# Kernel tuning notes

Hardware: AMD Instinct MI355X
Metric: run time of the kernel (lower is better)

The kernel has to match this reference:

```python
import jax, jax.numpy as jnp
import numpy as np

N_HEAD = 16
POSE = 5
YAW = 1
END_X, END_Y = 18, 32
THETA = 1000.0
LN_EPS = 1e-5

def compute_axial_cis(dim, end_x, end_y, theta):
    # Axial 2D rotary: dim is per-head dim; dim//4 freqs per spatial axis.
    n = dim // 4
    freqs = 1.0 / (theta ** (jnp.arange(0, dim, 4)[:n].astype(jnp.float32) / dim))
    t = jnp.arange(end_x * end_y, dtype=jnp.float32)
    t_x = t % end_x
    t_y = jnp.floor(t / end_x)
    ang = jnp.concatenate([t_x[:, None] * freqs[None, :], t_y[:, None] * freqs[None, :]], axis=-1)  # [L, dim//2]
    return jnp.cos(ang), jnp.sin(ang)

def apply_rotary(x, cos, sin):
    # x: [B,H,L,D]; complex pairing = consecutive (even, odd) lanes, as in view_as_complex
    xe, xo = x[..., 0::2], x[..., 1::2]
    oe = xe * cos - xo * sin
    oo = xe * sin + xo * cos
    return jnp.stack([oe, oo], axis=-1).reshape(x.shape)

def layernorm(z, g, b):
    m = jnp.mean(z, axis=-1, keepdims=True)
    v = jnp.mean(jnp.square(z - m), axis=-1, keepdims=True)
    return (z - m) * jax.lax.rsqrt(v + LN_EPS) * g + b

def setup_inputs() -> dict:
    key = jax.random.key(0)
    ks = jax.random.split(key, 8)
    B, T, C = 16, 582, 1024
    x = jax.random.normal(ks[0], (B, T, C), dtype=jnp.float32)
    # additive causal mask (0 keep / -1e9 masked), as a float attn_mask
    causal = jnp.tril(jnp.ones((T, T), dtype=jnp.float32))
    attn_mask = jnp.broadcast_to(jnp.where(causal > 0, 0.0, -1e9), (B, T, T))
    s = 0.02
    Wq = jax.random.normal(ks[1], (C, C), dtype=jnp.float32) * s
    Wk = jax.random.normal(ks[2], (C, C), dtype=jnp.float32) * s
    Wv = jax.random.normal(ks[3], (C, C), dtype=jnp.float32) * s
    Wo = jax.random.normal(ks[4], (C, C), dtype=jnp.float32) * s
    q_ln_g = jnp.ones((C,), jnp.float32); q_ln_b = jnp.zeros((C,), jnp.float32)
    k_ln_g = jnp.ones((C,), jnp.float32); k_ln_b = jnp.zeros((C,), jnp.float32)
    return {"x": x, "attn_mask": attn_mask, "Wq": Wq, "Wk": Wk, "Wv": Wv, "Wo": Wo,
            "q_ln_g": q_ln_g, "q_ln_b": q_ln_b, "k_ln_g": k_ln_g, "k_ln_b": k_ln_b}

def reference(x, attn_mask, Wq, Wk, Wv, Wo, q_ln_g, q_ln_b, k_ln_g, k_ln_b):
    B, T, C = x.shape
    H = N_HEAD
    D = C // H
    q = layernorm(x @ Wq.T, q_ln_g, q_ln_b)
    k = layernorm(x @ Wk.T, k_ln_g, k_ln_b)
    v = (x @ Wv.T).reshape(B, T, H, D).transpose(0, 2, 1, 3)
    q = q.reshape(B, T, H, D).transpose(0, 2, 1, 3)
    k = k.reshape(B, T, H, D).transpose(0, 2, 1, 3)
    prefix = POSE + YAW
    if T > prefix:  # static shape condition
        cos, sin = compute_axial_cis(D, END_X, END_Y, THETA)
        L = T - prefix
        cos, sin = cos[:L], sin[:L]  # [L, D//2]
        q = jnp.concatenate([q[:, :, :prefix], apply_rotary(q[:, :, prefix:], cos, sin)], axis=2)
        k = jnp.concatenate([k[:, :, :prefix], apply_rotary(k[:, :, prefix:], cos, sin)], axis=2)
    scale = 1.0 / jnp.sqrt(jnp.float32(D))
    scores = jnp.einsum("bhqd,bhkd->bhqk", q, k) * scale + attn_mask[:, None, :, :]
    att = jax.nn.softmax(scores, axis=-1)
    y = jnp.einsum("bhqk,bhkd->bhqd", att, v)
    y = y.transpose(0, 2, 1, 3).reshape(B, T, C)
    return y @ Wo.T
```

## Files before the change

### kernel.cpp

```cpp
#include <hip/hip_runtime.h>
#include <hip/hip_bf16.h>

typedef short bf16x8 __attribute__((ext_vector_type(8)));
typedef short bf16x4 __attribute__((ext_vector_type(4)));
typedef float f32x4  __attribute__((ext_vector_type(4)));

#define LDP 72

__device__ __forceinline__ float bits2f(short u) {
  return __uint_as_float(((unsigned int)(unsigned short)u) << 16);
}
__device__ __forceinline__ short f2bits(float f) {
  __hip_bfloat16 h = __float2bfloat16(f);
  return *reinterpret_cast<short*>(&h);
}
__device__ __forceinline__ void gld16(const short* g, short* l) {
  __builtin_amdgcn_global_load_lds(
      (const __attribute__((address_space(1))) void*)g,
      (__attribute__((address_space(3))) void*)l, 16, 0, 0);
}

__global__ __launch_bounds__(256)
void cvt_x_kernel(const float* __restrict__ src, short* __restrict__ dst, long n) {
  long i = ((long)blockIdx.x * 256 + threadIdx.x) * 4;
  if (i + 3 < n) {
    float4 v = *(const float4*)(src + i);
    bf16x4 o;
    o[0] = f2bits(v.x); o[1] = f2bits(v.y); o[2] = f2bits(v.z); o[3] = f2bits(v.w);
    *(bf16x4*)(dst + i) = o;
  }
}

__global__ __launch_bounds__(256)
void cvt_w_kernel(const float* __restrict__ w0, const float* __restrict__ w1,
                  const float* __restrict__ w2, const float* __restrict__ w3,
                  short* __restrict__ dst) {
  long i = ((long)blockIdx.x * 256 + threadIdx.x) * 4;
  int sel = (int)(i >> 20);
  const float* s = (sel == 0) ? w0 : (sel == 1) ? w1 : (sel == 2) ? w2 : w3;
  long off = i & ((1L << 20) - 1);
  float4 v = *(const float4*)(s + off);
  bf16x4 o;
  o[0] = f2bits(v.x); o[1] = f2bits(v.y); o[2] = f2bits(v.z); o[3] = f2bits(v.w);
  *(bf16x4*)(dst + i) = o;
}

template<int MODE>
__global__ __launch_bounds__(256)
void gemm_nt(const short* __restrict__ A, const short* __restrict__ Bm,
             float* __restrict__ OutF, short* __restrict__ Oq,
             short* __restrict__ Ok, short* __restrict__ Ov,
             int M, int K, int N, int T, int TPAD) {
  __shared__ short As[128 * 64];
  __shared__ short Bs[128 * 64];
  const int tid = threadIdx.x;
  const int w = tid >> 6, l = tid & 63;
  const int wr = w >> 1, wc = w & 1;
  const int lg = l >> 4, lo = l & 15;

  const int R = gridDim.x, C2 = gridDim.y;
  const int d = blockIdx.y * R + blockIdx.x;
  int r, c;
  if ((R & 7) == 1 && (C2 & 7) == 0) {
    const int x = d & 7, i = d >> 3;
    const int C8 = C2 >> 3;
    const int chunk = R * C8;
    const int b9 = R >> 3;
    const int rows0 = b9 + 1;
    if (x == 0) { c = i / rows0; r = i % rows0; }
    else {
      const int nb = b9 * C2;
      if (i < nb) { c = i / b9; r = rows0 + (x - 1) * b9 + i % b9; }
      else { int p = chunk + (x - 1) * C8 + (i - nb); c = p / rows0; r = p % rows0; }
    }
  } else { r = blockIdx.x; c = blockIdx.y; }
  const long row0 = (long)r * 128;
  const long col0 = (long)c * 128;

  const short* pa[4]; const short* pb[4]; short* la[4]; short* lb[4];
#pragma unroll
  for (int j = 0; j < 4; ++j) {
    const int ch = w * 4 + j;
    const int off = ch * 1024 + l * 16;
    const int row = off >> 7;
    const int lc  = (off & 127) ^ ((row & 7) << 4);
    long ga = row0 + row; if (ga > M - 1) ga = M - 1;
    pa[j] = &A[ga * K + (lc >> 1)];
    pb[j] = &Bm[(col0 + row) * K + (lc >> 1)];
    la[j] = &As[ch * 512];
    lb[j] = &Bs[ch * 512];
  }

  f32x4 acc[4][4] = {};

  for (int kt = 0; kt < K; kt += 64) {
    __syncthreads();
#pragma unroll
    for (int j = 0; j < 4; ++j) {
      gld16(pa[j] + kt, la[j]);
      gld16(pb[j] + kt, lb[j]);
    }
    __syncthreads();
    bf16x8 af[4][2], bfr[4][2];
#pragma unroll
    for (int mi = 0; mi < 4; ++mi)
#pragma unroll
      for (int ks = 0; ks < 2; ++ks) {
        int pe = (ks * 32 + lg * 8) ^ ((lo & 7) << 3);
        af[mi][ks] = *(const bf16x8*)(&As[(wr * 64 + mi * 16 + lo) * 64 + pe]);
      }
#pragma unroll
    for (int ni = 0; ni < 4; ++ni)
#pragma unroll
      for (int ks = 0; ks < 2; ++ks) {
        int pe = (ks * 32 + lg * 8) ^ ((lo & 7) << 3);
        bfr[ni][ks] = *(const bf16x8*)(&Bs[(wc * 64 + ni * 16 + lo) * 64 + pe]);
      }
#pragma unroll
    for (int mi = 0; mi < 4; ++mi)
#pragma unroll
      for (int ni = 0; ni < 4; ++ni)
#pragma unroll
        for (int ks = 0; ks < 2; ++ks)
          acc[mi][ni] = __builtin_amdgcn_mfma_f32_16x16x32_bf16(af[mi][ks], bfr[ni][ks], acc[mi][ni], 0, 0, 0);
  }

#pragma unroll
  for (int mi = 0; mi < 4; ++mi) {
#pragma unroll
    for (int rr = 0; rr < 4; ++rr) {
      long m = row0 + wr * 64 + mi * 16 + lg * 4 + rr;
      if (m >= M) continue;
#pragma unroll
      for (int ni = 0; ni < 4; ++ni) {
        long n = col0 + wc * 64 + ni * 16 + lo;
        float v = acc[mi][ni][rr];
        if constexpr (MODE == 2) {
          OutF[m * (long)N + n] = v;
        } else {
          if (n < 1024) {
            Oq[m * 1024 + n] = f2bits(v);
          } else if (n < 2048) {
            Ok[m * 1024 + (n - 1024)] = f2bits(v);
          } else {
            long b = m / T, t = m - b * T;
            long nn = n - 2048, h = nn >> 6, dd = nn & 63;
            Ov[((b * 16 + h) * 64 + dd) * TPAD + t] = f2bits(v);
          }
        }
      }
    }
  }
}

__global__ __launch_bounds__(256)
void ln_rope_kernel(const short* __restrict__ qpre, const short* __restrict__ kpre,
                    const float* __restrict__ qg, const float* __restrict__ qb2,
                    const float* __restrict__ kg, const float* __restrict__ kb2,
                    short* __restrict__ qa, short* __restrict__ ka, int T) {
  const int row = blockIdx.x;
  const short* in; const float *g, *be; short* out;
  if (blockIdx.y == 0) { in = qpre; g = qg; be = qb2; out = qa; }
  else                 { in = kpre; g = kg; be = kb2; out = ka; }
  const int tid = threadIdx.x;
  const int c0 = tid * 4;

  bf16x4 xv = *(const bf16x4*)(&in[(long)row * 1024 + c0]);
  float xf[4];
  float s = 0.f, sq = 0.f;
#pragma unroll
  for (int i = 0; i < 4; ++i) { xf[i] = bits2f(xv[i]); s += xf[i]; sq += xf[i] * xf[i]; }
#pragma unroll
  for (int o = 1; o < 64; o <<= 1) { s += __shfl_xor(s, o); sq += __shfl_xor(sq, o); }
  __shared__ float red[8];
  const int w = tid >> 6, l = tid & 63;
  if (l == 0) { red[w] = s; red[4 + w] = sq; }
  __syncthreads();
  s  = red[0] + red[1] + red[2] + red[3];
  sq = red[4] + red[5] + red[6] + red[7];
  const float mean = s * (1.0f / 1024.0f);
  const float var  = sq * (1.0f / 1024.0f) - mean * mean;
  const float rstd = rsqrtf(var + 1e-5f);

  float4 gv = *(const float4*)(&g[c0]);
  float4 bv = *(const float4*)(&be[c0]);
  float z[4];
  z[0] = (xf[0] - mean) * rstd * gv.x + bv.x;
  z[1] = (xf[1] - mean) * rstd * gv.y + bv.y;
  z[2] = (xf[2] - mean) * rstd * gv.z + bv.z;
  z[3] = (xf[3] - mean) * rstd * gv.w + bv.w;

  const int t = row % T;
  const int p = t - 6;
  if (p >= 0) {
    const float tx = (float)(p % 18);
    const float ty = (float)(p / 18);
    const int jbase = (c0 & 63) >> 1;
#pragma unroll
    for (int q2 = 0; q2 < 2; ++q2) {
      const int jj = jbase + q2;
      const int i  = jj & 15;
      const float freq = exp2f(-(float)i * 0.6228615177913804f);
      const float ang  = ((jj < 16) ? tx : ty) * freq;
      float sv, cv;
      sincosf(ang, &sv, &cv);
      const float xe = z[q2 * 2], xo = z[q2 * 2 + 1];
      z[q2 * 2]     = xe * cv - xo * sv;
      z[q2 * 2 + 1] = xe * sv + xo * cv;
    }
  }
  const long b = row / T;
  const int h = c0 >> 6, d = c0 & 63;
  bf16x4 ov;
#pragma unroll
  for (int i = 0; i < 4; ++i) ov[i] = f2bits(z[i]);
  *(bf16x4*)(&out[(((b * 16 + h) * T) + t) * 64 + d]) = ov;
}

__global__ __launch_bounds__(256)
void attn_kernel(const short* __restrict__ Q, const short* __restrict__ Kk,
                 const short* __restrict__ Vt, short* __restrict__ Y,
                 int T, int TPAD) {
  __shared__ short Ps[4][16 * LDP];
  const int tid = threadIdx.x;
  const int w = tid >> 6, l = tid & 63, lg = l >> 4, lo = l & 15;
  const int qb = gridDim.x - 1 - blockIdx.x;
  const int bh = blockIdx.y;
  const int b = bh >> 4, h = bh & 15;
  const long qbase = (long)bh * T * 64;
  const long vbase = (long)bh * 64;
  short* Pw = &Ps[w][0];

  const long qrow_l = qb * 64 + w * 16 + lo;
  bf16x8 qf[2];
  qf[0] = *(const bf16x8*)(&Q[qbase + qrow_l * 64 + lg * 8]);
  qf[1] = *(const bf16x8*)(&Q[qbase + qrow_l * 64 + 32 + lg * 8]);

  float mrow[4], lsum[4];
  f32x4 oacc[4] = {};
#pragma unroll
  for (int r = 0; r < 4; ++r) { mrow[r] = -3e38f; lsum[r] = 0.f; }
  const float SCL = 0.125f * 1.44269504f;
  const int nkt = qb + 1;

  for (int kt = 0; kt < nkt; ++kt) {
    bf16x8 kfr[4][2], vf[4][2];
#pragma unroll
    for (int ni = 0; ni < 4; ++ni)
#pragma unroll
      for (int kk = 0; kk < 2; ++kk)
        kfr[ni][kk] = *(const bf16x8*)(&Kk[qbase + (long)(kt * 64 + ni * 16 + lo) * 64 + kk * 32 + lg * 8]);
#pragma unroll
    for (int ni = 0; ni < 4; ++ni)
#pragma unroll
      for (int kk = 0; kk < 2; ++kk)
        vf[ni][kk] = *(const bf16x8*)(&Vt[(vbase + ni * 16 + lo) * TPAD + kt * 64 + kk * 32 + lg * 8]);

    f32x4 sf[4] = {};
#pragma unroll
    for (int ni = 0; ni < 4; ++ni)
#pragma unroll
      for (int kk = 0; kk < 2; ++kk)
        sf[ni] = __builtin_amdgcn_mfma_f32_16x16x32_bf16(qf[kk], kfr[ni][kk], sf[ni], 0, 0, 0);

    float pm[4][4], tmax[4];
#pragma unroll
    for (int r = 0; r < 4; ++r) tmax[r] = -3e38f;
#pragma unroll
    for (int ni = 0; ni < 4; ++ni)
#pragma unroll
      for (int r = 0; r < 4; ++r) {
        int key  = kt * 64 + ni * 16 + lo;
        int qrow = qb * 64 + w * 16 + lg * 4 + r;
        float sv = sf[ni][r] * SCL;
        if (key > qrow || key >= T) sv = -3e38f;
        pm[ni][r] = sv;
        tmax[r] = fmaxf(tmax[r], sv);
      }
#pragma unroll
    for (int r = 0; r < 4; ++r)
#pragma unroll
      for (int o = 1; o < 16; o <<= 1) tmax[r] = fmaxf(tmax[r], __shfl_xor(tmax[r], o));

    bool need = !__all(tmax[0] <= mrow[0] && tmax[1] <= mrow[1] &&
                       tmax[2] <= mrow[2] && tmax[3] <= mrow[3]);
    if (need) {
#pragma unroll
      for (int r = 0; r < 4; ++r) {
        float mn = fmaxf(mrow[r], tmax[r]);
        float fsc = exp2f(mrow[r] - mn);
        mrow[r] = mn;
        lsum[r] *= fsc;
#pragma unroll
        for (int ni = 0; ni < 4; ++ni) oacc[ni][r] *= fsc;
      }
    }
    float psum[4] = {0.f, 0.f, 0.f, 0.f};
#pragma unroll
    for (int ni = 0; ni < 4; ++ni)
#pragma unroll
      for (int r = 0; r < 4; ++r) {
        float pv = exp2f(pm[ni][r] - mrow[r]);
        pm[ni][r] = pv;
        psum[r] += pv;
      }
#pragma unroll
    for (int r = 0; r < 4; ++r) {
#pragma unroll
      for (int o = 1; o < 16; o <<= 1) psum[r] += __shfl_xor(psum[r], o);
      lsum[r] += psum[r];
    }

#pragma unroll
    for (int ni = 0; ni < 4; ++ni)
#pragma unroll
      for (int r = 0; r < 4; ++r)
        Pw[(lg * 4 + r) * LDP + ni * 16 + lo] = f2bits(pm[ni][r]);

#pragma unroll
    for (int kk = 0; kk < 2; ++kk) {
      bf16x8 pf = *(const bf16x8*)(&Pw[lo * LDP + kk * 32 + lg * 8]);
#pragma unroll
      for (int ni = 0; ni < 4; ++ni)
        oacc[ni] = __builtin_amdgcn_mfma_f32_16x16x32_bf16(pf, vf[ni][kk], oacc[ni], 0, 0, 0);
    }
  }

#pragma unroll
  for (int r = 0; r < 4; ++r) {
    int tq = qb * 64 + w * 16 + lg * 4 + r;
    if (tq >= T) continue;
    float inv = 1.0f / lsum[r];
#pragma unroll
    for (int ni = 0; ni < 4; ++ni) {
      float o = oacc[ni][r] * inv;
      Y[((long)b * T + tq) * 1024 + h * 64 + ni * 16 + lo] = f2bits(o);
    }
  }
}

extern "C" void kernel_launch(void* const* d_in, const int* in_sizes, int n_in,
                              void* d_out, int out_size, void* d_ws, size_t ws_size,
                              hipStream_t stream) {
  const float* x   = (const float*)d_in[0];
  const float* Wq  = (const float*)d_in[2];
  const float* Wk  = (const float*)d_in[3];
  const float* Wv  = (const float*)d_in[4];
  const float* Wo  = (const float*)d_in[5];
  const float* qg  = (const float*)d_in[6];
  const float* qb2 = (const float*)d_in[7];
  const float* kg  = (const float*)d_in[8];
  const float* kb2 = (const float*)d_in[9];

  const int B = 16, T = 582, C = 1024;
  const int M = B * T;
  const int TPAD = 584;

  short* ws = (short*)d_ws;
  const long E  = (long)M * C;
  const long EV = (long)B * 16 * 64 * TPAD;
  short* xb   = ws;
  short* qpre = ws + E;
  short* kpre = ws + 2 * E;
  short* ka   = ws + 3 * E;
  short* vat  = ws + 4 * E;
  short* wb   = ws + 4 * E + EV + 1024;
  short* qa   = xb;
  short* y    = qpre;
  float* out  = (float*)d_out;
  (void)ws_size; (void)in_sizes; (void)n_in; (void)out_size;

  const long WE = 1L << 20;

  cvt_x_kernel<<<(int)(E / 4 / 256), 256, 0, stream>>>(x, xb, E);
  cvt_w_kernel<<<(int)(4 * WE / 4 / 256), 256, 0, stream>>>(Wq, Wk, Wv, Wo, wb);

  dim3 gqkv((M + 127) / 128, 3072 / 128);
  gemm_nt<3><<<gqkv, 256, 0, stream>>>(xb, wb, nullptr, qpre, kpre, vat, M, C, 3072, T, TPAD);
  ln_rope_kernel<<<dim3(M, 2), 256, 0, stream>>>(qpre, kpre, qg, qb2, kg, kb2, qa, ka, T);
  attn_kernel<<<dim3((T + 63) / 64, B * 16), 256, 0, stream>>>(qa, ka, vat, y, T, TPAD);
  dim3 gout((M + 127) / 128, C / 128);
  gemm_nt<2><<<gout, 256, 0, stream>>>(y, wb + 3 * WE, out, nullptr, nullptr, nullptr, M, C, C, T, TPAD);
}
```

Measured before the change: 293.2 us.

## Merge conversion kernels, drop GEMM tile swizzle, compute softmax row sums via MFMA

The separate x and weight bf16 conversion kernels are merged into one launch, which removes a launch and its tail. The custom XCD-aware block remapping in the GEMM is removed in favour of plain blockIdx tiling. In attention, the per-row probability sum now comes from an extra MFMA against a ones vector, replacing the shuffle reductions. The sum is taken over the bf16-rounded probabilities, which slightly changes numerics, and the GEMM may lose L2 locality from the dropped swizzle.

```diff
diff --git a/kernel.cpp b/kernel.cpp
--- a/kernel.cpp
+++ b/kernel.cpp
@@ -21,28 +21,24 @@
 }
 
 __global__ __launch_bounds__(256)
-void cvt_x_kernel(const float* __restrict__ src, short* __restrict__ dst, long n) {
+void cvt_all_kernel(const float* __restrict__ x,
+                    const float* __restrict__ w0, const float* __restrict__ w1,
+                    const float* __restrict__ w2, const float* __restrict__ w3,
+                    short* __restrict__ xb, short* __restrict__ wb, long nx) {
   long i = ((long)blockIdx.x * 256 + threadIdx.x) * 4;
-  if (i + 3 < n) {
-    float4 v = *(const float4*)(src + i);
-    bf16x4 o;
-    o[0] = f2bits(v.x); o[1] = f2bits(v.y); o[2] = f2bits(v.z); o[3] = f2bits(v.w);
-    *(bf16x4*)(dst + i) = o;
-  }
-}
-
-__global__ __launch_bounds__(256)
-void cvt_w_kernel(const float* __restrict__ w0, const float* __restrict__ w1,
-                  const float* __restrict__ w2, const float* __restrict__ w3,
-                  short* __restrict__ dst) {
-  long i = ((long)blockIdx.x * 256 + threadIdx.x) * 4;
-  int sel = (int)(i >> 20);
-  const float* s = (sel == 0) ? w0 : (sel == 1) ? w1 : (sel == 2) ? w2 : w3;
-  long off = i & ((1L << 20) - 1);
+  const float* s; short* d; long off;
+  if (i < nx) { s = x; d = xb; off = i; }
+  else {
+    long j = i - nx;
+    int sel = (int)(j >> 20);
+    s = (sel == 0) ? w0 : (sel == 1) ? w1 : (sel == 2) ? w2 : w3;
+    d = wb + (j & ~((1L << 20) - 1));
+    off = j & ((1L << 20) - 1);
+  }
   float4 v = *(const float4*)(s + off);
   bf16x4 o;
   o[0] = f2bits(v.x); o[1] = f2bits(v.y); o[2] = f2bits(v.z); o[3] = f2bits(v.w);
-  *(bf16x4*)(dst + i) = o;
+  *(bf16x4*)(d + off) = o;
 }
 
 template<int MODE>
@@ -57,25 +53,8 @@
   const int w = tid >> 6, l = tid & 63;
   const int wr = w >> 1, wc = w & 1;
   const int lg = l >> 4, lo = l & 15;
-
-  const int R = gridDim.x, C2 = gridDim.y;
-  const int d = blockIdx.y * R + blockIdx.x;
-  int r, c;
-  if ((R & 7) == 1 && (C2 & 7) == 0) {
-    const int x = d & 7, i = d >> 3;
-    const int C8 = C2 >> 3;
-    const int chunk = R * C8;
-    const int b9 = R >> 3;
-    const int rows0 = b9 + 1;
-    if (x == 0) { c = i / rows0; r = i % rows0; }
-    else {
-      const int nb = b9 * C2;
-      if (i < nb) { c = i / b9; r = rows0 + (x - 1) * b9 + i % b9; }
-      else { int p = chunk + (x - 1) * C8 + (i - nb); c = p / rows0; r = p % rows0; }
-    }
-  } else { r = blockIdx.x; c = blockIdx.y; }
-  const long row0 = (long)r * 128;
-  const long col0 = (long)c * 128;
+  const long row0 = (long)blockIdx.x * 128;
+  const long col0 = (long)blockIdx.y * 128;
 
   const short* pa[4]; const short* pb[4]; short* la[4]; short* lb[4];
 #pragma unroll
@@ -128,13 +107,13 @@
 #pragma unroll
   for (int mi = 0; mi < 4; ++mi) {
 #pragma unroll
-    for (int rr = 0; rr < 4; ++rr) {
-      long m = row0 + wr * 64 + mi * 16 + lg * 4 + rr;
+    for (int r = 0; r < 4; ++r) {
+      long m = row0 + wr * 64 + mi * 16 + lg * 4 + r;
       if (m >= M) continue;
 #pragma unroll
       for (int ni = 0; ni < 4; ++ni) {
         long n = col0 + wc * 64 + ni * 16 + lo;
-        float v = acc[mi][ni][rr];
+        float v = acc[mi][ni][r];
         if constexpr (MODE == 2) {
           OutF[m * (long)N + n] = v;
         } else {
@@ -236,10 +215,14 @@
   qf[0] = *(const bf16x8*)(&Q[qbase + qrow_l * 64 + lg * 8]);
   qf[1] = *(const bf16x8*)(&Q[qbase + qrow_l * 64 + 32 + lg * 8]);
 
-  float mrow[4], lsum[4];
+  const short ONE = 0x3F80;
+  const bf16x8 ones = (bf16x8){ONE, ONE, ONE, ONE, ONE, ONE, ONE, ONE};
+
+  float mrow[4];
   f32x4 oacc[4] = {};
-#pragma unroll
-  for (int r = 0; r < 4; ++r) { mrow[r] = -3e38f; lsum[r] = 0.f; }
+  f32x4 lacc = {};
+#pragma unroll
+  for (int r = 0; r < 4; ++r) mrow[r] = -3e38f;
   const float SCL = 0.125f * 1.44269504f;
   const int nkt = qb + 1;
 
@@ -290,26 +273,16 @@
         float mn = fmaxf(mrow[r], tmax[r]);
         float fsc = exp2f(mrow[r] - mn);
         mrow[r] = mn;
-        lsum[r] *= fsc;
+        lacc[r] *= fsc;
 #pragma unroll
         for (int ni = 0; ni < 4; ++ni) oacc[ni][r] *= fsc;
       }
     }
-    float psum[4] = {0.f, 0.f, 0.f, 0.f};
-#pragma unroll
-    for (int ni = 0; ni < 4; ++ni)
-#pragma unroll
-      for (int r = 0; r < 4; ++r) {
-        float pv = exp2f(pm[ni][r] - mrow[r]);
-        pm[ni][r] = pv;
-        psum[r] += pv;
-      }
-#pragma unroll
-    for (int r = 0; r < 4; ++r) {
-#pragma unroll
-      for (int o = 1; o < 16; o <<= 1) psum[r] += __shfl_xor(psum[r], o);
-      lsum[r] += psum[r];
-    }
+#pragma unroll
+    for (int ni = 0; ni < 4; ++ni)
+#pragma unroll
+      for (int r = 0; r < 4; ++r)
+        pm[ni][r] = exp2f(pm[ni][r] - mrow[r]);
 
 #pragma unroll
     for (int ni = 0; ni < 4; ++ni)
@@ -320,6 +293,7 @@
 #pragma unroll
     for (int kk = 0; kk < 2; ++kk) {
       bf16x8 pf = *(const bf16x8*)(&Pw[lo * LDP + kk * 32 + lg * 8]);
+      lacc = __builtin_amdgcn_mfma_f32_16x16x32_bf16(pf, ones, lacc, 0, 0, 0);
 #pragma unroll
       for (int ni = 0; ni < 4; ++ni)
         oacc[ni] = __builtin_amdgcn_mfma_f32_16x16x32_bf16(pf, vf[ni][kk], oacc[ni], 0, 0, 0);
@@ -330,7 +304,7 @@
   for (int r = 0; r < 4; ++r) {
     int tq = qb * 64 + w * 16 + lg * 4 + r;
     if (tq >= T) continue;
-    float inv = 1.0f / lsum[r];
+    float inv = 1.0f / lacc[r];
 #pragma unroll
     for (int ni = 0; ni < 4; ++ni) {
       float o = oacc[ni][r] * inv;
@@ -372,8 +346,8 @@
 
   const long WE = 1L << 20;
 
-  cvt_x_kernel<<<(int)(E / 4 / 256), 256, 0, stream>>>(x, xb, E);
-  cvt_w_kernel<<<(int)(4 * WE / 4 / 256), 256, 0, stream>>>(Wq, Wk, Wv, Wo, wb);
+  const long NU = E / 4 + 4 * WE / 4;
+  cvt_all_kernel<<<(int)(NU / 256), 256, 0, stream>>>(x, Wq, Wk, Wv, Wo, xb, wb, E);
 
   dim3 gqkv((M + 127) / 128, 3072 / 128);
   gemm_nt<3><<<gqkv, 256, 0, stream>>>(xb, wb, nullptr, qpre, kpre, vat, M, C, 3072, T, TPAD);
```

Result: faster. 277.8 us (-5.2%).
